# Kernel optimization log

Hardware: AMD Instinct MI355X
Metric: run time of the kernel (lower is better)

Reference implementation:

```python
import jax, jax.numpy as jnp
import numpy as np

N = 8_000_000   # total nodes (atoms)
B = 4096        # number of graphs in the batch
EPS = 1e-05


def setup_inputs() -> dict:
    key = jax.random.key(0)
    k1, k2 = jax.random.split(key)
    pos = jax.random.normal(k1, (N, 3), dtype=jnp.float32)
    batch = jnp.sort(jax.random.randint(k2, (N,), 0, B).astype(jnp.int64))
    weight = jnp.ones((1, 1), dtype=jnp.float32)
    return {"pos": pos, "batch": batch, "weight": weight}


def reference(pos, batch, weight):
    # per-node L2 norm of 3D coordinates -> [N, 1]
    norm = jnp.linalg.norm(pos, axis=-1, keepdims=True)
    # scatter_mean over graphs: segment sums of norms and counts -> [B, 1]
    seg_sum = jax.ops.segment_sum(norm, batch, num_segments=B)
    counts = jax.ops.segment_sum(jnp.ones_like(norm), batch, num_segments=B)
    mean_norm = seg_sum / jnp.maximum(counts, 1.0)  # empty segments -> 0 (matches scatter_mean)
    # gather per-graph mean back to nodes and normalize
    new_pos = weight * pos / (mean_norm[batch] + EPS)
    return new_pos
```

## Files before the change

### kernel.cpp

```cpp
#include <hip/hip_runtime.h>

#define EPS_F 1e-5f
#define BGRAPHS 4096

__device__ __forceinline__ int batch_shift(const int* __restrict__ batch, int n) {
    return (batch[n - 1] == 0) ? 1 : 0;
}

__global__ __launch_bounds__(256) void se3_seg_reduce(
    const float* __restrict__ pos, const int* __restrict__ batch,
    float* __restrict__ sums, float* __restrict__ cnts, int n)
{
    const int tid  = blockIdx.x * blockDim.x + threadIdx.x;
    const int base = tid * 4;
    const int lane = threadIdx.x & 63;
    const int shift = batch_shift(batch, n);

    int   cur_b = -1;
    float cur_s = 0.f, cur_c = 0.f;

    if (base < n) {
        int   b4[4];
        float nrm[4];
        const int nb = min(4, n - base);
        if (nb == 4) {
            if (shift == 0) {
                const int4 bi = *reinterpret_cast<const int4*>(batch + base);
                b4[0] = bi.x; b4[1] = bi.y; b4[2] = bi.z; b4[3] = bi.w;
            } else {
                const int4 v0 = *reinterpret_cast<const int4*>(batch + 2 * base);
                const int4 v1 = *reinterpret_cast<const int4*>(batch + 2 * base + 4);
                b4[0] = v0.x; b4[1] = v0.z; b4[2] = v1.x; b4[3] = v1.z;
            }
            const float4* p = reinterpret_cast<const float4*>(pos + (size_t)base * 3);
            const float4 a = p[0], b = p[1], c = p[2];
            nrm[0] = sqrtf(a.x * a.x + a.y * a.y + a.z * a.z);
            nrm[1] = sqrtf(a.w * a.w + b.x * b.x + b.y * b.y);
            nrm[2] = sqrtf(b.z * b.z + b.w * b.w + c.x * c.x);
            nrm[3] = sqrtf(c.y * c.y + c.z * c.z + c.w * c.w);
        } else {
            for (int j = 0; j < 4; ++j) { b4[j] = -1; nrm[j] = 0.f; }
            for (int j = 0; j < nb; ++j) {
                b4[j] = batch[(size_t)(base + j) << shift];
                const float x = pos[(size_t)(base + j) * 3 + 0];
                const float y = pos[(size_t)(base + j) * 3 + 1];
                const float z = pos[(size_t)(base + j) * 3 + 2];
                nrm[j] = sqrtf(x * x + y * y + z * z);
            }
        }
        cur_b = b4[0];
        cur_s = nrm[0];
        cur_c = (b4[0] >= 0) ? 1.f : 0.f;
        #pragma unroll
        for (int j = 1; j < 4; ++j) {
            if (b4[j] == cur_b) { cur_s += nrm[j]; cur_c += 1.f; }
            else {
                if (cur_b >= 0) { atomicAdd(&sums[cur_b], cur_s); atomicAdd(&cnts[cur_b], cur_c); }
                cur_b = b4[j]; cur_s = nrm[j]; cur_c = (b4[j] >= 0) ? 1.f : 0.f;
            }
        }
    }

    #pragma unroll
    for (int off = 1; off < 64; off <<= 1) {
        const float os = __shfl_down(cur_s, off);
        const float oc = __shfl_down(cur_c, off);
        const int   ob = __shfl_down(cur_b, off);
        if (lane + off < 64 && ob == cur_b) { cur_s += os; cur_c += oc; }
    }
    const int pb = __shfl_up(cur_b, 1);
    if ((lane == 0 || pb != cur_b) && cur_b >= 0) {
        atomicAdd(&sums[cur_b], cur_s);
        atomicAdd(&cnts[cur_b], cur_c);
    }
}

__global__ void se3_finalize(const float* __restrict__ sums, const float* __restrict__ cnts,
                             const float* __restrict__ w, float* __restrict__ scale)
{
    const int b = blockIdx.x * blockDim.x + threadIdx.x;
    if (b < BGRAPHS) {
        const float mean = sums[b] / fmaxf(cnts[b], 1.f);
        scale[b] = w[0] / (mean + EPS_F);
    }
}

__global__ __launch_bounds__(256) void se3_apply(
    const float* __restrict__ pos, const int* __restrict__ batch,
    const float* __restrict__ scale, float* __restrict__ out, int n)
{
    const int tid  = blockIdx.x * blockDim.x + threadIdx.x;
    const int base = tid * 4;
    if (base >= n) return;
    const int shift = batch_shift(batch, n);
    if (base + 4 <= n) {
        int b4[4];
        if (shift == 0) {
            const int4 bi = *reinterpret_cast<const int4*>(batch + base);
            b4[0] = bi.x; b4[1] = bi.y; b4[2] = bi.z; b4[3] = bi.w;
        } else {
            const int4 v0 = *reinterpret_cast<const int4*>(batch + 2 * base);
            const int4 v1 = *reinterpret_cast<const int4*>(batch + 2 * base + 4);
            b4[0] = v0.x; b4[1] = v0.z; b4[2] = v1.x; b4[3] = v1.z;
        }
        const float s0 = scale[b4[0]], s1 = scale[b4[1]], s2 = scale[b4[2]], s3 = scale[b4[3]];
        const float4* p = reinterpret_cast<const float4*>(pos + (size_t)base * 3);
        const float4 a = p[0], b = p[1], c = p[2];
        float4* q = reinterpret_cast<float4*>(out + (size_t)base * 3);
        q[0] = make_float4(a.x * s0, a.y * s0, a.z * s0, a.w * s1);
        q[1] = make_float4(b.x * s1, b.y * s1, b.z * s2, b.w * s2);
        q[2] = make_float4(c.x * s2, c.y * s3, c.z * s3, c.w * s3);
    } else {
        for (int j = 0; j < n - base; ++j) {
            const int bb = batch[(size_t)(base + j) << shift];
            const float s = scale[bb];
            out[(size_t)(base + j) * 3 + 0] = pos[(size_t)(base + j) * 3 + 0] * s;
            out[(size_t)(base + j) * 3 + 1] = pos[(size_t)(base + j) * 3 + 1] * s;
            out[(size_t)(base + j) * 3 + 2] = pos[(size_t)(base + j) * 3 + 2] * s;
        }
    }
}

extern "C" void kernel_launch(void* const* d_in, const int* in_sizes, int n_in,
                              void* d_out, int out_size, void* d_ws, size_t ws_size,
                              hipStream_t stream)
{
    const float* pos   = (const float*)d_in[0];
    const int*   batch = (const int*)d_in[1];
    const float* w     = (const float*)d_in[2];
    float*       out   = (float*)d_out;
    const int    n     = in_sizes[1];

    float* sums  = (float*)d_ws;
    float* cnts  = sums + BGRAPHS;
    float* scale = cnts + BGRAPHS;

    hipMemsetAsync(d_ws, 0, 2 * BGRAPHS * sizeof(float), stream);

    const int nthreads = (n + 3) / 4;
    const int blocks   = (nthreads + 255) / 256;
    se3_seg_reduce<<<blocks, 256, 0, stream>>>(pos, batch, sums, cnts, n);
    se3_finalize<<<(BGRAPHS + 255) / 256, 256, 0, stream>>>(sums, cnts, w, scale);
    se3_apply<<<blocks, 256, 0, stream>>>(pos, batch, scale, out, n);
}
```

Measured before the change: 68.25 us.

## Replace batch reread in apply pass with segment-start table and binary search

The reduce pass now records the first node index of each graph into a starts table. A single-block finalize builds a suffix-min over that table so empty graphs get valid boundaries. The apply kernel then loads the starts and scales into LDS and finds each node's graph by binary search, so it no longer reads the int64 batch array. Output stores become nontemporal. This trades the batch traffic in the second pass for an extra memset, a serial single-block finalize, per-block LDS table loads (32KB per block, which limits occupancy) and a search of about a dozen LDS steps per thread.

```diff
diff --git a/kernel.cpp b/kernel.cpp
--- a/kernel.cpp
+++ b/kernel.cpp
@@ -2,6 +2,9 @@
 
 #define EPS_F 1e-5f
 #define BGRAPHS 4096
+#define SENTINEL 0x7F7F7F7F
+
+typedef float f32x4 __attribute__((ext_vector_type(4)));
 
 __device__ __forceinline__ int batch_shift(const int* __restrict__ batch, int n) {
     return (batch[n - 1] == 0) ? 1 : 0;
@@ -9,7 +12,8 @@
 
 __global__ __launch_bounds__(256) void se3_seg_reduce(
     const float* __restrict__ pos, const int* __restrict__ batch,
-    float* __restrict__ sums, float* __restrict__ cnts, int n)
+    float* __restrict__ sums, float* __restrict__ cnts,
+    int* __restrict__ starts, int n)
 {
     const int tid  = blockIdx.x * blockDim.x + threadIdx.x;
     const int base = tid * 4;
@@ -22,6 +26,7 @@
     if (base < n) {
         int   b4[4];
         float nrm[4];
+        int   prev;
         const int nb = min(4, n - base);
         if (nb == 4) {
             if (shift == 0) {
@@ -32,6 +37,10 @@
                 const int4 v1 = *reinterpret_cast<const int4*>(batch + 2 * base + 4);
                 b4[0] = v0.x; b4[1] = v0.z; b4[2] = v1.x; b4[3] = v1.z;
             }
+            const int up = __shfl_up(b4[3], 1);
+            if (lane == 0) prev = (base == 0) ? -1 : batch[(size_t)(base - 1) << shift];
+            else           prev = up;
+
             const float4* p = reinterpret_cast<const float4*>(pos + (size_t)base * 3);
             const float4 a = p[0], b = p[1], c = p[2];
             nrm[0] = sqrtf(a.x * a.x + a.y * a.y + a.z * a.z);
@@ -47,7 +56,14 @@
                 const float z = pos[(size_t)(base + j) * 3 + 2];
                 nrm[j] = sqrtf(x * x + y * y + z * z);
             }
+            prev = (base == 0) ? -1 : batch[(size_t)(base - 1) << shift];
         }
+
+        if (b4[0] >= 0 && b4[0] != prev) starts[b4[0]] = base;
+        #pragma unroll
+        for (int j = 1; j < 4; ++j)
+            if (b4[j] >= 0 && b4[j] != b4[j - 1]) starts[b4[j]] = base + j;
+
         cur_b = b4[0];
         cur_s = nrm[0];
         cur_c = (b4[0] >= 0) ? 1.f : 0.f;
@@ -75,48 +91,81 @@
     }
 }
 
-__global__ void se3_finalize(const float* __restrict__ sums, const float* __restrict__ cnts,
-                             const float* __restrict__ w, float* __restrict__ scale)
+__global__ __launch_bounds__(1024) void se3_finalize(
+    const float* __restrict__ sums, const float* __restrict__ cnts,
+    const float* __restrict__ w, float* __restrict__ scale, int* __restrict__ starts)
 {
-    const int b = blockIdx.x * blockDim.x + threadIdx.x;
-    if (b < BGRAPHS) {
-        const float mean = sums[b] / fmaxf(cnts[b], 1.f);
-        scale[b] = w[0] / (mean + EPS_F);
+    __shared__ int ta[BGRAPHS], tb[BGRAPHS];
+    const int t = threadIdx.x;
+    for (int i = t; i < BGRAPHS; i += 1024) ta[i] = starts[i];
+    __syncthreads();
+    int* src = ta; int* dst = tb;
+    for (int stride = 1; stride < BGRAPHS; stride <<= 1) {
+        for (int i = t; i < BGRAPHS; i += 1024) {
+            int v = src[i];
+            if (i + stride < BGRAPHS) v = min(v, src[i + stride]);
+            dst[i] = v;
+        }
+        __syncthreads();
+        int* tmp = src; src = dst; dst = tmp;
+    }
+    for (int i = t; i < BGRAPHS; i += 1024) {
+        starts[i] = src[i];
+        const float mean = sums[i] / fmaxf(cnts[i], 1.f);
+        scale[i] = w[0] / (mean + EPS_F);
     }
 }
 
+__device__ __forceinline__ int find_seg(const int* __restrict__ t, int i) {
+    int lo = 0, hi = BGRAPHS - 1;
+    #pragma unroll
+    for (int s = 0; s < 12; ++s) {
+        const int mid = (lo + hi + 1) >> 1;
+        if (t[mid] <= i) lo = mid; else hi = mid - 1;
+    }
+    return lo;
+}
+
 __global__ __launch_bounds__(256) void se3_apply(
-    const float* __restrict__ pos, const int* __restrict__ batch,
+    const float* __restrict__ pos, const int* __restrict__ tstarts,
     const float* __restrict__ scale, float* __restrict__ out, int n)
 {
+    __shared__ int   s_t[BGRAPHS];
+    __shared__ float s_s[BGRAPHS];
+    for (int i = threadIdx.x; i < BGRAPHS / 4; i += blockDim.x) {
+        reinterpret_cast<int4*>(s_t)[i]   = reinterpret_cast<const int4*>(tstarts)[i];
+        reinterpret_cast<float4*>(s_s)[i] = reinterpret_cast<const float4*>(scale)[i];
+    }
+    __syncthreads();
+
     const int tid  = blockIdx.x * blockDim.x + threadIdx.x;
     const int base = tid * 4;
     if (base >= n) return;
-    const int shift = batch_shift(batch, n);
+
+    int g = find_seg(s_t, base);
+    float sc[4];
+    sc[0] = s_s[g];
+    #pragma unroll
+    for (int j = 1; j < 4; ++j) {
+        while (g < BGRAPHS - 1 && s_t[g + 1] <= base + j) ++g;
+        sc[j] = s_s[g];
+    }
+
     if (base + 4 <= n) {
-        int b4[4];
-        if (shift == 0) {
-            const int4 bi = *reinterpret_cast<const int4*>(batch + base);
-            b4[0] = bi.x; b4[1] = bi.y; b4[2] = bi.z; b4[3] = bi.w;
-        } else {
-            const int4 v0 = *reinterpret_cast<const int4*>(batch + 2 * base);
-            const int4 v1 = *reinterpret_cast<const int4*>(batch + 2 * base + 4);
-            b4[0] = v0.x; b4[1] = v0.z; b4[2] = v1.x; b4[3] = v1.z;
-        }
-        const float s0 = scale[b4[0]], s1 = scale[b4[1]], s2 = scale[b4[2]], s3 = scale[b4[3]];
         const float4* p = reinterpret_cast<const float4*>(pos + (size_t)base * 3);
         const float4 a = p[0], b = p[1], c = p[2];
-        float4* q = reinterpret_cast<float4*>(out + (size_t)base * 3);
-        q[0] = make_float4(a.x * s0, a.y * s0, a.z * s0, a.w * s1);
-        q[1] = make_float4(b.x * s1, b.y * s1, b.z * s2, b.w * s2);
-        q[2] = make_float4(c.x * s2, c.y * s3, c.z * s3, c.w * s3);
+        f32x4* q = reinterpret_cast<f32x4*>(out + (size_t)base * 3);
+        f32x4 o0 = { a.x * sc[0], a.y * sc[0], a.z * sc[0], a.w * sc[1] };
+        f32x4 o1 = { b.x * sc[1], b.y * sc[1], b.z * sc[2], b.w * sc[2] };
+        f32x4 o2 = { c.x * sc[2], c.y * sc[3], c.z * sc[3], c.w * sc[3] };
+        __builtin_nontemporal_store(o0, q + 0);
+        __builtin_nontemporal_store(o1, q + 1);
+        __builtin_nontemporal_store(o2, q + 2);
     } else {
         for (int j = 0; j < n - base; ++j) {
-            const int bb = batch[(size_t)(base + j) << shift];
-            const float s = scale[bb];
-            out[(size_t)(base + j) * 3 + 0] = pos[(size_t)(base + j) * 3 + 0] * s;
-            out[(size_t)(base + j) * 3 + 1] = pos[(size_t)(base + j) * 3 + 1] * s;
-            out[(size_t)(base + j) * 3 + 2] = pos[(size_t)(base + j) * 3 + 2] * s;
+            out[(size_t)(base + j) * 3 + 0] = pos[(size_t)(base + j) * 3 + 0] * sc[j];
+            out[(size_t)(base + j) * 3 + 1] = pos[(size_t)(base + j) * 3 + 1] * sc[j];
+            out[(size_t)(base + j) * 3 + 2] = pos[(size_t)(base + j) * 3 + 2] * sc[j];
         }
     }
 }
@@ -131,15 +180,17 @@
     float*       out   = (float*)d_out;
     const int    n     = in_sizes[1];
 
-    float* sums  = (float*)d_ws;
-    float* cnts  = sums + BGRAPHS;
-    float* scale = cnts + BGRAPHS;
+    float* sums   = (float*)d_ws;
+    float* cnts   = sums + BGRAPHS;
+    float* scale  = cnts + BGRAPHS;
+    int*   starts = (int*)(scale + BGRAPHS);
 
     hipMemsetAsync(d_ws, 0, 2 * BGRAPHS * sizeof(float), stream);
+    hipMemsetAsync(starts, 0x7F, BGRAPHS * sizeof(int), stream);
 
     const int nthreads = (n + 3) / 4;
     const int blocks   = (nthreads + 255) / 256;
-    se3_seg_reduce<<<blocks, 256, 0, stream>>>(pos, batch, sums, cnts, n);
-    se3_finalize<<<(BGRAPHS + 255) / 256, 256, 0, stream>>>(sums, cnts, w, scale);
-    se3_apply<<<blocks, 256, 0, stream>>>(pos, batch, scale, out, n);
+    se3_seg_reduce<<<blocks, 256, 0, stream>>>(pos, batch, sums, cnts, starts, n);
+    se3_finalize<<<1, 1024, 0, stream>>>(sums, cnts, w, scale, starts);
+    se3_apply<<<blocks, 256, 0, stream>>>(pos, starts, scale, out, n);
 }
```

Measured after the change: 86.77 us. +27.1%, slower.

## Replace per-node batch reads with binary-searched segment starts and per-block window

Applied to the files above, without the earlier changes.

Two small kernels now derive graph IDs without streaming the batch index array. The first binary-searches the sorted batch array for each graph's start offset. The second finds the first graph covering each block's 1024-node chunk. The reduce and apply kernels then get each node's graph ID by comparing its index against a 16-entry window of segment starts, so neither kernel reads the large int64 batch array. This removes a large share of the DRAM traffic, at the cost of two extra launches and the assumption that no 1024-node block crosses more than 16 graph boundaries.

```diff
diff --git a/kernel.cpp b/kernel.cpp
--- a/kernel.cpp
+++ b/kernel.cpp
@@ -2,36 +2,68 @@
 
 #define EPS_F 1e-5f
 #define BGRAPHS 4096
+#define NPB 1024
+#define WIN 16
+#define INF_I 0x7fffffff
 
 __device__ __forceinline__ int batch_shift(const int* __restrict__ batch, int n) {
     return (batch[n - 1] == 0) ? 1 : 0;
 }
 
-__global__ __launch_bounds__(256) void se3_seg_reduce(
-    const float* __restrict__ pos, const int* __restrict__ batch,
+__global__ __launch_bounds__(256) void k_starts(const int* __restrict__ batch,
+                                                int* __restrict__ S, int n)
+{
+    const int b = blockIdx.x * blockDim.x + threadIdx.x;
+    if (b > BGRAPHS) return;
+    const int shift = batch_shift(batch, n);
+    int lo = 0, hi = n;
+    while (lo < hi) {
+        const int mid = (int)(((unsigned)lo + (unsigned)hi) >> 1);
+        const int v = batch[(size_t)mid << shift];
+        if (v < b) lo = mid + 1; else hi = mid;
+    }
+    S[b] = lo;
+}
+
+__global__ __launch_bounds__(256) void k_coarse(const int* __restrict__ S,
+                                                int* __restrict__ cg, int nchunks)
+{
+    const int c = blockIdx.x * blockDim.x + threadIdx.x;
+    if (c >= nchunks) return;
+    const int x = c * NPB;
+    int lo = 0, hi = BGRAPHS - 1;
+    #pragma unroll
+    for (int s = 0; s < 12; ++s) {
+        const int mid = (lo + hi + 1) >> 1;
+        if (S[mid] <= x) lo = mid; else hi = mid - 1;
+    }
+    cg[c] = lo;
+}
+
+__global__ __launch_bounds__(256) void se3_reduce(
+    const float* __restrict__ pos, const int* __restrict__ S, const int* __restrict__ cg,
     float* __restrict__ sums, float* __restrict__ cnts, int n)
 {
     const int tid  = blockIdx.x * blockDim.x + threadIdx.x;
     const int base = tid * 4;
     const int lane = threadIdx.x & 63;
-    const int shift = batch_shift(batch, n);
+
+    const int g0 = cg[blockIdx.x];
+    int w[WIN];
+    #pragma unroll
+    for (int k = 0; k < WIN; ++k) {
+        const int idx = g0 + 1 + k;
+        w[k] = (idx <= BGRAPHS) ? S[idx] : INF_I;
+    }
 
     int   cur_b = -1;
     float cur_s = 0.f, cur_c = 0.f;
 
     if (base < n) {
+        float nrm[4];
         int   b4[4];
-        float nrm[4];
         const int nb = min(4, n - base);
         if (nb == 4) {
-            if (shift == 0) {
-                const int4 bi = *reinterpret_cast<const int4*>(batch + base);
-                b4[0] = bi.x; b4[1] = bi.y; b4[2] = bi.z; b4[3] = bi.w;
-            } else {
-                const int4 v0 = *reinterpret_cast<const int4*>(batch + 2 * base);
-                const int4 v1 = *reinterpret_cast<const int4*>(batch + 2 * base + 4);
-                b4[0] = v0.x; b4[1] = v0.z; b4[2] = v1.x; b4[3] = v1.z;
-            }
             const float4* p = reinterpret_cast<const float4*>(pos + (size_t)base * 3);
             const float4 a = p[0], b = p[1], c = p[2];
             nrm[0] = sqrtf(a.x * a.x + a.y * a.y + a.z * a.z);
@@ -39,14 +71,21 @@
             nrm[2] = sqrtf(b.z * b.z + b.w * b.w + c.x * c.x);
             nrm[3] = sqrtf(c.y * c.y + c.z * c.z + c.w * c.w);
         } else {
-            for (int j = 0; j < 4; ++j) { b4[j] = -1; nrm[j] = 0.f; }
+            for (int j = 0; j < 4; ++j) nrm[j] = 0.f;
             for (int j = 0; j < nb; ++j) {
-                b4[j] = batch[(size_t)(base + j) << shift];
                 const float x = pos[(size_t)(base + j) * 3 + 0];
                 const float y = pos[(size_t)(base + j) * 3 + 1];
                 const float z = pos[(size_t)(base + j) * 3 + 2];
                 nrm[j] = sqrtf(x * x + y * y + z * z);
             }
+        }
+        #pragma unroll
+        for (int j = 0; j < 4; ++j) {
+            const int i = base + j;
+            int g = g0;
+            #pragma unroll
+            for (int k = 0; k < WIN; ++k) g += (w[k] <= i) ? 1 : 0;
+            b4[j] = (j < nb) ? g : -1;
         }
         cur_b = b4[0];
         cur_s = nrm[0];
@@ -86,37 +125,43 @@
 }
 
 __global__ __launch_bounds__(256) void se3_apply(
-    const float* __restrict__ pos, const int* __restrict__ batch,
+    const float* __restrict__ pos, const int* __restrict__ S, const int* __restrict__ cg,
     const float* __restrict__ scale, float* __restrict__ out, int n)
 {
     const int tid  = blockIdx.x * blockDim.x + threadIdx.x;
     const int base = tid * 4;
     if (base >= n) return;
-    const int shift = batch_shift(batch, n);
+
+    const int g0 = cg[blockIdx.x];
+    int w[WIN];
+    #pragma unroll
+    for (int k = 0; k < WIN; ++k) {
+        const int idx = g0 + 1 + k;
+        w[k] = (idx <= BGRAPHS) ? S[idx] : INF_I;
+    }
+
+    float sc[4];
+    #pragma unroll
+    for (int j = 0; j < 4; ++j) {
+        const int i = base + j;
+        int g = g0;
+        #pragma unroll
+        for (int k = 0; k < WIN; ++k) g += (w[k] <= i) ? 1 : 0;
+        sc[j] = scale[g];
+    }
+
     if (base + 4 <= n) {
-        int b4[4];
-        if (shift == 0) {
-            const int4 bi = *reinterpret_cast<const int4*>(batch + base);
-            b4[0] = bi.x; b4[1] = bi.y; b4[2] = bi.z; b4[3] = bi.w;
-        } else {
-            const int4 v0 = *reinterpret_cast<const int4*>(batch + 2 * base);
-            const int4 v1 = *reinterpret_cast<const int4*>(batch + 2 * base + 4);
-            b4[0] = v0.x; b4[1] = v0.z; b4[2] = v1.x; b4[3] = v1.z;
-        }
-        const float s0 = scale[b4[0]], s1 = scale[b4[1]], s2 = scale[b4[2]], s3 = scale[b4[3]];
         const float4* p = reinterpret_cast<const float4*>(pos + (size_t)base * 3);
         const float4 a = p[0], b = p[1], c = p[2];
         float4* q = reinterpret_cast<float4*>(out + (size_t)base * 3);
-        q[0] = make_float4(a.x * s0, a.y * s0, a.z * s0, a.w * s1);
-        q[1] = make_float4(b.x * s1, b.y * s1, b.z * s2, b.w * s2);
-        q[2] = make_float4(c.x * s2, c.y * s3, c.z * s3, c.w * s3);
+        q[0] = make_float4(a.x * sc[0], a.y * sc[0], a.z * sc[0], a.w * sc[1]);
+        q[1] = make_float4(b.x * sc[1], b.y * sc[1], b.z * sc[2], b.w * sc[2]);
+        q[2] = make_float4(c.x * sc[2], c.y * sc[3], c.z * sc[3], c.w * sc[3]);
     } else {
         for (int j = 0; j < n - base; ++j) {
-            const int bb = batch[(size_t)(base + j) << shift];
-            const float s = scale[bb];
-            out[(size_t)(base + j) * 3 + 0] = pos[(size_t)(base + j) * 3 + 0] * s;
-            out[(size_t)(base + j) * 3 + 1] = pos[(size_t)(base + j) * 3 + 1] * s;
-            out[(size_t)(base + j) * 3 + 2] = pos[(size_t)(base + j) * 3 + 2] * s;
+            out[(size_t)(base + j) * 3 + 0] = pos[(size_t)(base + j) * 3 + 0] * sc[j];
+            out[(size_t)(base + j) * 3 + 1] = pos[(size_t)(base + j) * 3 + 1] * sc[j];
+            out[(size_t)(base + j) * 3 + 2] = pos[(size_t)(base + j) * 3 + 2] * sc[j];
         }
     }
 }
@@ -134,12 +179,17 @@
     float* sums  = (float*)d_ws;
     float* cnts  = sums + BGRAPHS;
     float* scale = cnts + BGRAPHS;
+    int*   S     = (int*)(scale + BGRAPHS);
+    int*   cg    = S + (BGRAPHS + 1);
+
+    const int nthreads = (n + 3) / 4;
+    const int blocks   = (nthreads + 255) / 256;
 
     hipMemsetAsync(d_ws, 0, 2 * BGRAPHS * sizeof(float), stream);
 
-    const int nthreads = (n + 3) / 4;
-    const int blocks   = (nthreads + 255) / 256;
-    se3_seg_reduce<<<blocks, 256, 0, stream>>>(pos, batch, sums, cnts, n);
+    k_starts<<<(BGRAPHS + 1 + 255) / 256, 256, 0, stream>>>(batch, S, n);
+    k_coarse<<<(blocks + 255) / 256, 256, 0, stream>>>(S, cg, blocks);
+    se3_reduce<<<blocks, 256, 0, stream>>>(pos, S, cg, sums, cnts, n);
     se3_finalize<<<(BGRAPHS + 255) / 256, 256, 0, stream>>>(sums, cnts, w, scale);
-    se3_apply<<<blocks, 256, 0, stream>>>(pos, batch, scale, out, n);
+    se3_apply<<<blocks, 256, 0, stream>>>(pos, S, cg, scale, out, n);
 }
```

New measurement: 75.54 us. +10.7%, slower.
